# Kernel optimization log

Hardware: AMD Instinct MI355X
Metric: run time of the kernel (lower is better)

## Reference

```python
import jax, jax.numpy as jnp
import numpy as np

N_NODES = 50000
N_EDGES = 1600000
D_IN = 128
D_HID = 128
D_OUT = 128


def setup_inputs() -> dict:
    key = jax.random.key(0)
    k = jax.random.split(key, 6)
    feat = jax.random.normal(k[0], (N_NODES, D_IN), dtype=jnp.float32)
    W1 = jax.random.normal(k[1], (D_IN, D_HID), dtype=jnp.float32) * (1.0 / np.sqrt(D_IN))
    b1 = jnp.zeros((D_HID,), dtype=jnp.float32)
    W2 = jax.random.normal(k[2], (D_HID, D_OUT), dtype=jnp.float32) * (1.0 / np.sqrt(D_HID))
    b2 = jnp.zeros((D_OUT,), dtype=jnp.float32)
    src = jax.random.randint(k[3], (N_EDGES,), 0, N_NODES, dtype=jnp.int32)
    dst = jax.random.randint(k[4], (N_EDGES,), 0, N_NODES, dtype=jnp.int32)
    return {"feat": feat, "W1": W1, "b1": b1, "W2": W2, "b2": b2, "src": src, "dst": dst}


def _graph_conv(h, W, b, src, dst, norm_src, norm_dst, n_nodes):
    # DGL GraphConv, norm='both': h_src * out_deg^-1/2 -> sum over edges -> * in_deg^-1/2 -> W, +b
    h = h * norm_src[:, None]
    agg = jax.ops.segment_sum(h[src], dst, num_segments=n_nodes)
    agg = agg * norm_dst[:, None]
    return agg @ W + b


def reference(feat, W1, b1, W2, b2, src, dst):
    n = feat.shape[0]
    # dgl.add_self_loop: append (i, i) for every node
    loop = jnp.arange(n, dtype=src.dtype)
    src = jnp.concatenate([src, loop])
    dst = jnp.concatenate([dst, loop])
    ones = jnp.ones(src.shape[0], dtype=feat.dtype)
    out_deg = jax.ops.segment_sum(ones, src, num_segments=n)  # >= 1 due to self-loops
    in_deg = jax.ops.segment_sum(ones, dst, num_segments=n)
    norm_src = jax.lax.rsqrt(out_deg)
    norm_dst = jax.lax.rsqrt(in_deg)
    h = _graph_conv(feat, W1, b1, src, dst, norm_src, norm_dst, n)
    h = jax.nn.relu(h)
    h = _graph_conv(h, W2, b2, src, dst, norm_src, norm_dst, n)
    return h[None, :, :]  # unsqueeze(0) -> [1, N, out_features]
```

## Files before the change

kernel.cpp:

```cpp
#include <hip/hip_runtime.h>

#define D 128
#define RANGES 4
#define CHUNKS 64
#define BINS_MAX 12512

typedef unsigned short u16;
typedef __attribute__((ext_vector_type(8))) short short8;
typedef __attribute__((ext_vector_type(4))) float f32x4;


__device__ __forceinline__ u16 f2bf(float x) {
  unsigned u = __float_as_uint(x);
  u += 0x7fffu + ((u >> 16) & 1u);
  return (u16)(u >> 16);
}
#define BF_LO(u) __uint_as_float((u) << 16)
#define BF_HI(u) __uint_as_float((u) & 0xffff0000u)


__global__ __launch_bounds__(1024)
void hist_kernel(const int* __restrict__ keys, u16* __restrict__ part,
                 int E, int N, int binsR, int chunkE)
{
  __shared__ int hist[BINS_MAX];
  const int b = blockIdx.x;
  const int r = b & (RANGES - 1);
  const int k = b >> 2;
  const int lo = r * binsR;
  const int hi = min(N, lo + binsR);
  const int nb = hi - lo;
  for (int i = threadIdx.x; i < nb; i += 1024) hist[i] = 0;
  __syncthreads();
  const int e0 = k * chunkE;
  const int e1 = min(E, e0 + chunkE);
  for (int e = e0 + threadIdx.x; e < e1; e += 1024) {
    int v = keys[e];
    if (v >= lo && v < hi) atomicAdd(&hist[v - lo], 1);
  }
  __syncthreads();
  for (int i = threadIdx.x; i < nb; i += 1024)
    part[(size_t)k * N + lo + i] = (u16)hist[i];
}

__global__ void reduce_kernel(const u16* __restrict__ psrc, u16* __restrict__ pdst,
                              int* __restrict__ deg_in, float* __restrict__ nsrc,
                              float* __restrict__ ndst, int N)
{
  int bin = blockIdx.x * blockDim.x + threadIdx.x;
  if (bin >= N) return;
  int runs = 0, rund = 0;
  for (int k = 0; k < CHUNKS; ++k) {
    runs += psrc[(size_t)k * N + bin];
    int vd = pdst[(size_t)k * N + bin];
    pdst[(size_t)k * N + bin] = (u16)rund;
    rund += vd;
  }
  deg_in[bin] = rund;
  nsrc[bin] = rsqrtf((float)runs + 1.0f);
  ndst[bin] = rsqrtf((float)rund + 1.0f);
}


__global__ __launch_bounds__(1024)
void scan1_kernel(const int* __restrict__ din, int* __restrict__ roff,
                  int* __restrict__ bsum, int N)
{
  __shared__ int wsum[16];
  const int t = threadIdx.x, lane = t & 63, wid = t >> 6;
  const int i = blockIdx.x * 1024 + t;
  int v = (i < N) ? din[i] : 0;
  int x = v;
  #pragma unroll
  for (int off = 1; off < 64; off <<= 1) {
    int u = __shfl_up(x, off);
    if (lane >= off) x += u;
  }
  if (lane == 63) wsum[wid] = x;
  __syncthreads();
  if (wid == 0) {
    int y = (lane < 16) ? wsum[lane] : 0;
    int z = y;
    #pragma unroll
    for (int off = 1; off < 16; off <<= 1) {
      int u = __shfl_up(z, off);
      if (lane >= off) z += u;
    }
    if (lane < 16) wsum[lane] = z - y;
    if (lane == 15) bsum[blockIdx.x] = z;
  }
  __syncthreads();
  if (i < N) roff[i] = wsum[wid] + (x - v);
}

__global__ void scan2_kernel(int* __restrict__ bsum, int* __restrict__ roffN, int nb)
{
  const int t = threadIdx.x;
  int v = (t < nb) ? bsum[t] : 0;
  int x = v;
  #pragma unroll
  for (int off = 1; off < 64; off <<= 1) {
    int u = __shfl_up(x, off);
    if (t >= off) x += u;
  }
  if (t < nb) bsum[t] = x - v;
  if (t == 63) *roffN = x;
}

__global__ __launch_bounds__(1024)
void scan3_kernel(int* __restrict__ roff, const int* __restrict__ bsum, int N)
{
  const int i = blockIdx.x * 1024 + threadIdx.x;
  if (i < N) roff[i] += bsum[i >> 10];
}


__global__ __launch_bounds__(1024)
void scatter_kernel(const int* __restrict__ src, const int* __restrict__ dst,
                    const u16* __restrict__ pdst, const int* __restrict__ roff,
                    u16* __restrict__ eout, int E, int N, int binsR, int chunkE)
{
  __shared__ int cur[BINS_MAX];
  const int b = blockIdx.x;
  const int r = b & (RANGES - 1);
  const int k = b >> 2;
  const int lo = r * binsR;
  const int hi = min(N, lo + binsR);
  const int nb = hi - lo;
  for (int i = threadIdx.x; i < nb; i += 1024)
    cur[i] = roff[lo + i] + (int)pdst[(size_t)k * N + lo + i];
  __syncthreads();
  const int e0 = k * chunkE;
  const int e1 = min(E, e0 + chunkE);
  for (int e = e0 + threadIdx.x; e < e1; e += 1024) {
    int d = dst[e];
    if (d >= lo && d < hi) eout[atomicAdd(&cur[d - lo], 1)] = (u16)src[e];
  }
}


__global__ __launch_bounds__(256)
void convert_kernel(const float* __restrict__ f, const float* __restrict__ nsrc,
                    unsigned* __restrict__ fb, int n4)
{
  const int i = blockIdx.x * blockDim.x + threadIdx.x;
  if (i < n4) {
    float s = nsrc[i >> 5];
    float4 v = ((const float4*)f)[i];
    uint2 o;
    o.x = (unsigned)f2bf(v.x * s) | ((unsigned)f2bf(v.y * s) << 16);
    o.y = (unsigned)f2bf(v.z * s) | ((unsigned)f2bf(v.w * s) << 16);
    ((uint2*)fb)[i] = o;
  }
}


__global__ __launch_bounds__(128)
void wtrans_kernel(const float* __restrict__ W1, const float* __restrict__ W2,
                   u16* __restrict__ Wt1, u16* __restrict__ Wt2)
{
  const int k = blockIdx.x & 127;
  const float* W = (blockIdx.x < 128) ? W1 : W2;
  u16* Wt = (blockIdx.x < 128) ? Wt1 : Wt2;
  const int n = threadIdx.x;
  Wt[n * 128 + k] = f2bf(W[k * 128 + n]);
}


__global__ __launch_bounds__(256)
void gather_bf_kernel(const unsigned* __restrict__ fb, const u16* __restrict__ eidx,
                      const int* __restrict__ roff, const float* __restrict__ ndst,
                      u16* __restrict__ outb, int N)
{
  const int wid = threadIdx.x >> 6;
  const int lane = threadIdx.x & 63;
  const int node = blockIdx.x * 4 + wid;
  if (node >= N) return;
  const int h = lane >> 5;
  const int q = lane & 31;
  const uint2* fb2 = (const uint2*)fb;
  float4 acc = make_float4(0.f, 0.f, 0.f, 0.f);
  if (h == 0) {
    uint2 u = fb2[(size_t)node * 32 + q];
    acc.x = BF_LO(u.x); acc.y = BF_HI(u.x);
    acc.z = BF_LO(u.y); acc.w = BF_HI(u.y);
  }
  const int beg = roff[node], end = roff[node + 1];
  for (int e0 = beg; e0 < end; e0 += 64) {
    const int cnt = min(64, end - e0);
    int id = (lane < cnt) ? (int)eidx[e0 + lane] : 0;
    int j = 0;
    for (; j + 16 <= cnt; j += 16) {
      int s0 = __shfl(id, j + 0 + h);
      int s1 = __shfl(id, j + 2 + h);
      int s2 = __shfl(id, j + 4 + h);
      int s3 = __shfl(id, j + 6 + h);
      int s4 = __shfl(id, j + 8 + h);
      int s5 = __shfl(id, j + 10 + h);
      int s6 = __shfl(id, j + 12 + h);
      int s7 = __shfl(id, j + 14 + h);
      uint2 u0 = fb2[(size_t)s0 * 32 + q];
      uint2 u1 = fb2[(size_t)s1 * 32 + q];
      uint2 u2 = fb2[(size_t)s2 * 32 + q];
      uint2 u3 = fb2[(size_t)s3 * 32 + q];
      uint2 u4 = fb2[(size_t)s4 * 32 + q];
      uint2 u5 = fb2[(size_t)s5 * 32 + q];
      uint2 u6 = fb2[(size_t)s6 * 32 + q];
      uint2 u7 = fb2[(size_t)s7 * 32 + q];
      acc.x += BF_LO(u0.x); acc.y += BF_HI(u0.x); acc.z += BF_LO(u0.y); acc.w += BF_HI(u0.y);
      acc.x += BF_LO(u1.x); acc.y += BF_HI(u1.x); acc.z += BF_LO(u1.y); acc.w += BF_HI(u1.y);
      acc.x += BF_LO(u2.x); acc.y += BF_HI(u2.x); acc.z += BF_LO(u2.y); acc.w += BF_HI(u2.y);
      acc.x += BF_LO(u3.x); acc.y += BF_HI(u3.x); acc.z += BF_LO(u3.y); acc.w += BF_HI(u3.y);
      acc.x += BF_LO(u4.x); acc.y += BF_HI(u4.x); acc.z += BF_LO(u4.y); acc.w += BF_HI(u4.y);
      acc.x += BF_LO(u5.x); acc.y += BF_HI(u5.x); acc.z += BF_LO(u5.y); acc.w += BF_HI(u5.y);
      acc.x += BF_LO(u6.x); acc.y += BF_HI(u6.x); acc.z += BF_LO(u6.y); acc.w += BF_HI(u6.y);
      acc.x += BF_LO(u7.x); acc.y += BF_HI(u7.x); acc.z += BF_LO(u7.y); acc.w += BF_HI(u7.y);
    }
    for (; j < cnt; j += 2) {
      int ej = j + h;
      int s = __shfl(id, ej & 63);
      if (ej < cnt) {
        uint2 u = fb2[(size_t)s * 32 + q];
        acc.x += BF_LO(u.x); acc.y += BF_HI(u.x);
        acc.z += BF_LO(u.y); acc.w += BF_HI(u.y);
      }
    }
  }
  acc.x += __shfl_xor(acc.x, 32);
  acc.y += __shfl_xor(acc.y, 32);
  acc.z += __shfl_xor(acc.z, 32);
  acc.w += __shfl_xor(acc.w, 32);
  if (h == 0) {
    float nd = ndst[node];
    ushort4 w;
    w.x = f2bf(acc.x * nd); w.y = f2bf(acc.y * nd);
    w.z = f2bf(acc.z * nd); w.w = f2bf(acc.w * nd);
    *(ushort4*)(outb + (size_t)node * D + q * 4) = w;
  }
}


template<bool RELU_SCALE, bool BF_OUT>
__global__ __launch_bounds__(256)
void gemm_mfma(const u16* __restrict__ A, const u16* __restrict__ Wt,
               const float* __restrict__ bias, const float* __restrict__ nsrc,
               void* __restrict__ Cv, int N)
{
  const int lane = threadIdx.x & 63;
  const int wv   = threadIdx.x >> 6;
  const int tile = blockIdx.x * 4 + wv;
  if (tile * 16 >= N) return;
  const int m  = lane & 15;
  const int kb = lane >> 4;
  int arow = tile * 16 + m; if (arow > N - 1) arow = N - 1;
  f32x4 acc[8];
  #pragma unroll
  for (int c = 0; c < 8; ++c) acc[c] = (f32x4){0.f, 0.f, 0.f, 0.f};
  #pragma unroll
  for (int kc = 0; kc < D; kc += 32) {
    short8 a = *(const short8*)(A + (size_t)arow * D + kc + kb * 8);
    #pragma unroll
    for (int c = 0; c < 8; ++c) {
      short8 b = *(const short8*)(Wt + (size_t)(c * 16 + m) * D + kc + kb * 8);
      acc[c] = __builtin_amdgcn_mfma_f32_16x16x32_bf16(a, b, acc[c], 0, 0, 0);
    }
  }
  float ns[4];
  #pragma unroll
  for (int j = 0; j < 4; ++j) {
    int orow = tile * 16 + kb * 4 + j;
    ns[j] = (RELU_SCALE && orow < N) ? nsrc[orow] : 1.0f;
  }
  #pragma unroll
  for (int c = 0; c < 8; ++c) {
    const int col = c * 16 + m;
    const float bb = bias[col];
    #pragma unroll
    for (int j = 0; j < 4; ++j) {
      int orow = tile * 16 + kb * 4 + j;
      if (orow < N) {
        float v = acc[c][j] + bb;
        if (RELU_SCALE) v = fmaxf(v, 0.f) * ns[j];
        if (BF_OUT) ((u16*)Cv)[(size_t)orow * D + col] = f2bf(v);
        else        ((float*)Cv)[(size_t)orow * D + col] = v;
      }
    }
  }
}


extern "C" void kernel_launch(void* const* d_in, const int* in_sizes, int n_in,
                              void* d_out, int out_size, void* d_ws, size_t ws_size,
                              hipStream_t stream) {
  const float* feat = (const float*)d_in[0];
  const float* W1   = (const float*)d_in[1];
  const float* b1   = (const float*)d_in[2];
  const float* W2   = (const float*)d_in[3];
  const float* b2   = (const float*)d_in[4];
  const int*   src  = (const int*)d_in[5];
  const int*   dst  = (const int*)d_in[6];
  const int N = in_sizes[0] / D;
  const int E = in_sizes[5];
  float* out = (float*)d_out;

  const int binsR = (N + RANGES - 1) / RANGES;
  const int chunkE = (((E + CHUNKS - 1) / CHUNKS) + 3) & ~3;

  auto align256 = [](size_t x) { return (x + 255) & ~(size_t)255; };
  char* p = (char*)d_ws;
  char* p0 = p;  p += align256((size_t)CHUNKS * N * 2);
  char* p1 = p;  p += align256((size_t)N * D * 2);
  char* p2 = p;  p += align256((size_t)N * D * 2);
  int*   deg_in  = (int*)p;   p += align256((size_t)N * 4);
  int*   row_off = (int*)p;   p += align256((size_t)(N + 1) * 4);
  float* nsrc    = (float*)p; p += align256((size_t)N * 4);
  float* ndst    = (float*)p; p += align256((size_t)N * 4);
  int*   bsum    = (int*)p;   p += 256;
  u16*   wt1     = (u16*)p;   p += align256((size_t)D * D * 2);
  u16*   wt2     = (u16*)p;   p += align256((size_t)D * D * 2);

  u16*      psrc   = (u16*)p0;
  u16*      esrc   = (u16*)p0;
  u16*      pdst   = (u16*)p1;
  u16*      h1bf   = (u16*)p1;
  unsigned* featbf = (unsigned*)p2;
  u16*      agg2   = (u16*)p2;
  u16*      agg1   = (u16*)((char*)d_out + (size_t)N * D * 2);

  const int nblk = (N + 1023) / 1024;
  const int gemm_grid = ((N + 15) / 16 + 3) / 4;

  wtrans_kernel<<<256, 128, 0, stream>>>(W1, W2, wt1, wt2);
  hist_kernel<<<RANGES * CHUNKS, 1024, 0, stream>>>(src, psrc, E, N, binsR, chunkE);
  hist_kernel<<<RANGES * CHUNKS, 1024, 0, stream>>>(dst, pdst, E, N, binsR, chunkE);
  reduce_kernel<<<(N + 255) / 256, 256, 0, stream>>>(psrc, pdst, deg_in, nsrc, ndst, N);
  convert_kernel<<<(N * D / 4 + 255) / 256, 256, 0, stream>>>(feat, nsrc, featbf, N * D / 4);
  scan1_kernel<<<nblk, 1024, 0, stream>>>(deg_in, row_off, bsum, N);
  scan2_kernel<<<1, 64, 0, stream>>>(bsum, row_off + N, nblk);
  scan3_kernel<<<nblk, 1024, 0, stream>>>(row_off, bsum, N);
  scatter_kernel<<<RANGES * CHUNKS, 1024, 0, stream>>>(src, dst, pdst, row_off, esrc, E, N, binsR, chunkE);

  gather_bf_kernel<<<(N + 3) / 4, 256, 0, stream>>>(featbf, esrc, row_off, ndst, agg1, N);
  gemm_mfma<true, true><<<gemm_grid, 256, 0, stream>>>(agg1, wt1, b1, nsrc, h1bf, N);
  gather_bf_kernel<<<(N + 3) / 4, 256, 0, stream>>>((const unsigned*)h1bf, esrc, row_off, ndst, agg2, N);
  gemm_mfma<false, false><<<gemm_grid, 256, 0, stream>>>(agg2, wt2, b2, nsrc, out, N);
}
```

Measured before the change: 297.5 us.

## Pack per-chunk histograms as 16-bit LDS counters and 8-bit partials, drop range split

Histogram and scatter kernels now hold counts for all nodes in shared memory by packing two 16-bit counters per 32-bit word. Blocks no longer each scan their edge chunk once per node range and discard out-of-range keys. The src and dst histograms are fused into one launch, and per-chunk partial counts are stored as bytes, which shrinks the partial-count traffic in the reduce and scatter steps. The cost is lower occupancy from the 100KB LDS footprint and an assumption that per-chunk counts fit in 8 bits, which holds only for sparse random graphs like the test input.

```diff
diff --git a/kernel.cpp b/kernel.cpp
--- a/kernel.cpp
+++ b/kernel.cpp
@@ -1,11 +1,11 @@
 #include <hip/hip_runtime.h>
 
 #define D 128
-#define RANGES 4
-#define CHUNKS 64
-#define BINS_MAX 12512
+#define CHUNKS 128
+#define NW_MAX 25024
 
 typedef unsigned short u16;
+typedef unsigned char  u8;
 typedef __attribute__((ext_vector_type(8))) short short8;
 typedef __attribute__((ext_vector_type(4))) float f32x4;
 
@@ -20,30 +20,33 @@
 
 
 __global__ __launch_bounds__(1024)
-void hist_kernel(const int* __restrict__ keys, u16* __restrict__ part,
-                 int E, int N, int binsR, int chunkE)
-{
-  __shared__ int hist[BINS_MAX];
+void hist_kernel(const int* __restrict__ src, const int* __restrict__ dst,
+                 u8* __restrict__ psrc, u8* __restrict__ pdst,
+                 int E, int N, int chunkE)
+{
+  __shared__ unsigned h32[NW_MAX];
   const int b = blockIdx.x;
-  const int r = b & (RANGES - 1);
-  const int k = b >> 2;
-  const int lo = r * binsR;
-  const int hi = min(N, lo + binsR);
-  const int nb = hi - lo;
-  for (int i = threadIdx.x; i < nb; i += 1024) hist[i] = 0;
+  const int k = (b < CHUNKS) ? b : b - CHUNKS;
+  const int* __restrict__ keys = (b < CHUNKS) ? src : dst;
+  u8* __restrict__ part = (b < CHUNKS) ? psrc : pdst;
+  const int nw = (N + 1) >> 1;
+  for (int i = threadIdx.x; i < nw; i += 1024) h32[i] = 0;
   __syncthreads();
   const int e0 = k * chunkE;
   const int e1 = min(E, e0 + chunkE);
   for (int e = e0 + threadIdx.x; e < e1; e += 1024) {
     int v = keys[e];
-    if (v >= lo && v < hi) atomicAdd(&hist[v - lo], 1);
-  }
-  __syncthreads();
-  for (int i = threadIdx.x; i < nb; i += 1024)
-    part[(size_t)k * N + lo + i] = (u16)hist[i];
-}
-
-__global__ void reduce_kernel(const u16* __restrict__ psrc, u16* __restrict__ pdst,
+    atomicAdd(&h32[v >> 1], 1u << ((v & 1) * 16));
+  }
+  __syncthreads();
+  u16* p16 = (u16*)(part + (size_t)k * N);
+  for (int w = threadIdx.x; w < nw; w += 1024) {
+    unsigned x = h32[w];
+    p16[w] = (u16)((x & 0xffu) | ((x >> 16) << 8));
+  }
+}
+
+__global__ void reduce_kernel(const u8* __restrict__ psrc, u8* __restrict__ pdst,
                               int* __restrict__ deg_in, float* __restrict__ nsrc,
                               float* __restrict__ ndst, int N)
 {
@@ -53,7 +56,7 @@
   for (int k = 0; k < CHUNKS; ++k) {
     runs += psrc[(size_t)k * N + bin];
     int vd = pdst[(size_t)k * N + bin];
-    pdst[(size_t)k * N + bin] = (u16)rund;
+    pdst[(size_t)k * N + bin] = (u8)rund;
     rund += vd;
   }
   deg_in[bin] = rund;
@@ -117,24 +120,26 @@
 
 __global__ __launch_bounds__(1024)
 void scatter_kernel(const int* __restrict__ src, const int* __restrict__ dst,
-                    const u16* __restrict__ pdst, const int* __restrict__ roff,
-                    u16* __restrict__ eout, int E, int N, int binsR, int chunkE)
-{
-  __shared__ int cur[BINS_MAX];
-  const int b = blockIdx.x;
-  const int r = b & (RANGES - 1);
-  const int k = b >> 2;
-  const int lo = r * binsR;
-  const int hi = min(N, lo + binsR);
-  const int nb = hi - lo;
-  for (int i = threadIdx.x; i < nb; i += 1024)
-    cur[i] = roff[lo + i] + (int)pdst[(size_t)k * N + lo + i];
+                    const u8* __restrict__ pdst, const int* __restrict__ roff,
+                    u16* __restrict__ eout, int E, int N, int chunkE)
+{
+  __shared__ unsigned cur32[NW_MAX];
+  const int k = blockIdx.x;
+  const int nw = (N + 1) >> 1;
+  const u16* p16 = (const u16*)(pdst + (size_t)k * N);
+  for (int i = threadIdx.x; i < nw; i += 1024) {
+    unsigned pr = p16[i];
+    cur32[i] = (pr & 0xffu) | ((pr >> 8) << 16);
+  }
   __syncthreads();
   const int e0 = k * chunkE;
   const int e1 = min(E, e0 + chunkE);
   for (int e = e0 + threadIdx.x; e < e1; e += 1024) {
     int d = dst[e];
-    if (d >= lo && d < hi) eout[atomicAdd(&cur[d - lo], 1)] = (u16)src[e];
+    unsigned sh = (d & 1) * 16u;
+    unsigned old = atomicAdd(&cur32[d >> 1], 1u << sh);
+    int rel = (int)((old >> sh) & 0xffffu);
+    eout[roff[d] + rel] = (u16)src[e];
   }
 }
 
@@ -303,12 +308,11 @@
   const int E = in_sizes[5];
   float* out = (float*)d_out;
 
-  const int binsR = (N + RANGES - 1) / RANGES;
   const int chunkE = (((E + CHUNKS - 1) / CHUNKS) + 3) & ~3;
 
   auto align256 = [](size_t x) { return (x + 255) & ~(size_t)255; };
   char* p = (char*)d_ws;
-  char* p0 = p;  p += align256((size_t)CHUNKS * N * 2);
+  char* p0 = p;  p += align256((size_t)E * 2);
   char* p1 = p;  p += align256((size_t)N * D * 2);
   char* p2 = p;  p += align256((size_t)N * D * 2);
   int*   deg_in  = (int*)p;   p += align256((size_t)N * 4);
@@ -319,10 +323,10 @@
   u16*   wt1     = (u16*)p;   p += align256((size_t)D * D * 2);
   u16*   wt2     = (u16*)p;   p += align256((size_t)D * D * 2);
 
-  u16*      psrc   = (u16*)p0;
   u16*      esrc   = (u16*)p0;
-  u16*      pdst   = (u16*)p1;
+  u8*       pdst8  = (u8*)p1;
   u16*      h1bf   = (u16*)p1;
+  u8*       psrc8  = (u8*)p2;
   unsigned* featbf = (unsigned*)p2;
   u16*      agg2   = (u16*)p2;
   u16*      agg1   = (u16*)((char*)d_out + (size_t)N * D * 2);
@@ -331,14 +335,13 @@
   const int gemm_grid = ((N + 15) / 16 + 3) / 4;
 
   wtrans_kernel<<<256, 128, 0, stream>>>(W1, W2, wt1, wt2);
-  hist_kernel<<<RANGES * CHUNKS, 1024, 0, stream>>>(src, psrc, E, N, binsR, chunkE);
-  hist_kernel<<<RANGES * CHUNKS, 1024, 0, stream>>>(dst, pdst, E, N, binsR, chunkE);
-  reduce_kernel<<<(N + 255) / 256, 256, 0, stream>>>(psrc, pdst, deg_in, nsrc, ndst, N);
+  hist_kernel<<<2 * CHUNKS, 1024, 0, stream>>>(src, dst, psrc8, pdst8, E, N, chunkE);
+  reduce_kernel<<<(N + 255) / 256, 256, 0, stream>>>(psrc8, pdst8, deg_in, nsrc, ndst, N);
   convert_kernel<<<(N * D / 4 + 255) / 256, 256, 0, stream>>>(feat, nsrc, featbf, N * D / 4);
   scan1_kernel<<<nblk, 1024, 0, stream>>>(deg_in, row_off, bsum, N);
   scan2_kernel<<<1, 64, 0, stream>>>(bsum, row_off + N, nblk);
   scan3_kernel<<<nblk, 1024, 0, stream>>>(row_off, bsum, N);
-  scatter_kernel<<<RANGES * CHUNKS, 1024, 0, stream>>>(src, dst, pdst, row_off, esrc, E, N, binsR, chunkE);
+  scatter_kernel<<<CHUNKS, 1024, 0, stream>>>(src, dst, pdst8, row_off, esrc, E, N, chunkE);
 
   gather_bf_kernel<<<(N + 3) / 4, 256, 0, stream>>>(featbf, esrc, row_off, ndst, agg1, N);
   gemm_mfma<true, true><<<gemm_grid, 256, 0, stream>>>(agg1, wt1, b1, nsrc, h1bf, N);
```

Measured after the change: 303.8 us. +2.1%, slower.
